# Optimization experiments

Measured on AMD Instinct MI355X. Metric: run time of the kernel, lower is better.

Reference implementation:

```python
import jax, jax.numpy as jnp
import numpy as np

# 3x3 window roll offsets, row-major as in PatchShift2D.shift_content
SHIFTS = [(1, 1), (1, 0), (1, -1), (0, 1), (0, 0), (0, -1), (-1, 1), (-1, 0), (-1, -1)]
NUM_WIN = 9


def patch_shift(x, inv):
    # x: [B, T, H, W, C]; pad C up to multiple of 9 and H,W by 1, roll each
    # of the 9 channel groups by a distinct (h, w) offset, then crop back.
    B, T, H, W, C = x.shape
    Ch = int(np.ceil(C / NUM_WIN) * NUM_WIN)
    xp = jnp.pad(x, ((0, 0), (0, 0), (1, 1), (1, 1), (0, Ch - C)))
    m = -1 if inv else 1
    parts = jnp.split(xp, NUM_WIN, axis=-1)
    shifted = [jnp.roll(p, (m * sh, m * sw), axis=(2, 3))
               for p, (sh, sw) in zip(parts, SHIFTS)]
    return jnp.concatenate(shifted, axis=-1)[:, :, 1:H + 1, 1:W + 1, :C]


def _gelu(v):
    return jax.nn.gelu(v, approximate=False)  # torch nn.GELU default (erf)


def setup_inputs() -> dict:
    key = jax.random.key(0)
    ks = jax.random.split(key, 14)
    B, T, H, W, C = 2, 8, 56, 56, 512
    HID = 1024
    s = 0.02
    return {
        "x": jax.random.normal(ks[0], (B, T, H, W, C), dtype=jnp.float32),
        "fc_w": s * jax.random.normal(ks[1], (C, HID), dtype=jnp.float32),
        "fc_b": jnp.zeros((HID,), jnp.float32),
        "fc1_w": s * jax.random.normal(ks[2], (HID, C), dtype=jnp.float32),
        "fc1_b": jnp.zeros((C,), jnp.float32),
        "fc2_w": s * jax.random.normal(ks[3], (HID, C), dtype=jnp.float32),
        "fc2_b": jnp.zeros((C,), jnp.float32),
        "rw1_w": s * jax.random.normal(ks[4], (C, C // 4), dtype=jnp.float32),
        "rw1_b": jnp.zeros((C // 4,), jnp.float32),
        "rw2_w": s * jax.random.normal(ks[5], (C // 4, 2 * C), dtype=jnp.float32),
        "rw2_b": jnp.zeros((2 * C,), jnp.float32),
        "proj_w": s * jax.random.normal(ks[6], (C, C), dtype=jnp.float32),
        "proj_b": jnp.zeros((C,), jnp.float32),
    }


def reference(x, fc_w, fc_b, fc1_w, fc1_b, fc2_w, fc2_b,
              rw1_w, rw1_b, rw2_w, rw2_b, proj_w, proj_b):
    B, T, H, W, C = x.shape
    xh = _gelu(x @ fc_w + fc_b)                                  # [B,T,H,W,HID]
    h = patch_shift(_gelu(patch_shift(xh, False) @ fc1_w + fc1_b), True)  # [B,T,H,W,C]
    w = _gelu(xh @ fc2_w + fc2_b)                                 # [B,T,H,W,C]
    a = (h + w).mean(axis=(1, 2, 3))                              # [B,C]
    a = _gelu(a @ rw1_w + rw1_b) @ rw2_w + rw2_b                  # [B,2C]
    a = jax.nn.softmax(a.reshape(B, C, 2).transpose(2, 0, 1), axis=0)  # [2,B,C]
    a = a[:, :, None, None, None, :]                              # [2,B,1,1,1,C]
    out = h * a[0] + w * a[1]
    return out @ proj_w + proj_b
```

## Files before the change

### kernel.cpp

```cpp
#include <hip/hip_runtime.h>
#include <hip/hip_bf16.h>
#include <stdint.h>


typedef __attribute__((ext_vector_type(8))) short short8;
typedef __attribute__((ext_vector_type(4))) float floatx4;
typedef unsigned int uint;
typedef unsigned short ushort;

#define NTOK   50176
#define HWIMG  3136

__device__ __align__(64) uint g_zpage[16];

__device__ __forceinline__ float gelu_exact(float v) {
    return 0.5f * v * (1.0f + erff(v * 0.70710678118654752440f));
}
__device__ __forceinline__ float gelu_fast(float v) {
    float u = v * (0.7978845608f + 0.0356774081f * v * v);
    return v * __builtin_amdgcn_rcpf(1.0f + __expf(-2.0f * u));
}

__device__ __forceinline__ int shift_h(int g) { return 1 - g / 3; }
__device__ __forceinline__ int shift_w(int g) { return 1 - g % 3; }

typedef const __attribute__((address_space(1))) uint* gas_ptr;
typedef __attribute__((address_space(3))) uint* las_ptr;

__device__ __forceinline__ void async_copy16(const void* g, void* l) {
    gas_ptr gp = (gas_ptr)(uintptr_t)g;
    las_ptr lp = (las_ptr)(uint32_t)(uintptr_t)l;
    __builtin_amdgcn_global_load_lds(gp, lp, 16, 0, 0);
}

template <int EPI, bool SHIFTA>
__global__ __launch_bounds__(256) void gemm_bt(
    const __hip_bfloat16* __restrict__ A,
    const __hip_bfloat16* __restrict__ Bt,
    const float* __restrict__ bias,
    void* __restrict__ Cout,
    float* __restrict__ ssum, int N, int K)
{
    __shared__ __align__(16) __hip_bfloat16 As[2 * 128 * 32];
    __shared__ __align__(16) __hip_bfloat16 Bs[2 * 128 * 32];

    const int t    = threadIdx.x;
    const int lane = t & 63;
    const int wave = t >> 6;
    const int wm   = wave >> 1;
    const int wn   = wave & 1;

    const int nbn  = gridDim.x;
    const int flat = blockIdx.y * nbn + blockIdx.x;
    const int xcd  = flat & 7;
    const int j    = flat >> 3;
    const int jd   = j / nbn;
    const int bm   = xcd * 49 + jd;
    const int bn   = j - jd * nbn;

    const int ar0 = bm * 128 + (t >> 2);
    const int ar1 = ar0 + 64;
    const int ac  = (t & 3) * 8;

    const __hip_bfloat16* ga0 = A  + (size_t)ar0 * K + ac;
    const __hip_bfloat16* ga1 = ga0 + (size_t)64 * K;
    const __hip_bfloat16* gb0 = Bt + (size_t)(bn * 128 + (t >> 2)) * K + ac;
    const __hip_bfloat16* gb1 = gb0 + (size_t)64 * K;

    floatx4 acc[4][4] = {};

    const int kq = (lane >> 4) * 8;
    const int ml = lane & 15;

    if constexpr (!SHIFTA) {
        auto stage = [&](int buf) {
            __hip_bfloat16* lA = &As[buf * 4096 + t * 8];
            __hip_bfloat16* lB = &Bs[buf * 4096 + t * 8];
            async_copy16(ga0, lA);
            async_copy16(ga1, lA + 2048);
            async_copy16(gb0, lB);
            async_copy16(gb1, lB + 2048);
            ga0 += 32; ga1 += 32; gb0 += 32; gb1 += 32;
        };

        const int nt = K >> 5;
        stage(0);
        for (int tt = 0; tt < nt; ++tt) {
            const int cur = tt & 1;
            if (tt + 1 < nt) {
                stage(cur ^ 1);
                asm volatile("s_waitcnt vmcnt(4)" ::: "memory");
            } else {
                asm volatile("s_waitcnt vmcnt(0)" ::: "memory");
            }
            __builtin_amdgcn_s_barrier();
            asm volatile("" ::: "memory");

            const int ab = cur * 4096;
            short8 af[4], bf[4];
#pragma unroll
            for (int i = 0; i < 4; i++) {
                af[i] = *(const short8*)&As[ab + (wm * 64 + i * 16 + ml) * 32 + kq];
                bf[i] = *(const short8*)&Bs[ab + (wn * 64 + i * 16 + ml) * 32 + kq];
            }
#pragma unroll
            for (int mi = 0; mi < 4; mi++)
#pragma unroll
                for (int ni = 0; ni < 4; ni++)
                    acc[mi][ni] = __builtin_amdgcn_mfma_f32_16x16x32_bf16(
                        af[mi], bf[ni], acc[mi][ni], 0, 0, 0);

            asm volatile("" ::: "memory");
            __builtin_amdgcn_s_barrier();
        }
    } else {
        const int rem0 = ar0 % HWIMG, rem1 = ar1 % HWIMG;
        const int oh0 = rem0 / 56, ow0 = rem0 - oh0 * 56;
        const int oh1 = rem1 / 56, ow1 = rem1 - oh1 * 56;
        const __hip_bfloat16* zsrc = (const __hip_bfloat16*)g_zpage;

        auto stageS = [&](int buf, int tx, bool& strad,
                          uint4& lo0, uint4& hi0, uint4& lo1, uint4& hi1) {
            const int c0 = tx * 32 + ac;
            const int gl = c0 / 114;
            const int gh = (c0 + 7) / 114;
            const int shl = shift_h(gl), swl = shift_w(gl);
            const int offl = shl * 56 + swl;
            const bool v0 = ((unsigned)(oh0 - shl) < 56u) && ((unsigned)(ow0 - swl) < 56u);
            const bool v1 = ((unsigned)(oh1 - shl) < 56u) && ((unsigned)(ow1 - swl) < 56u);
            strad = (gl != gh);
            const __hip_bfloat16* p0 = zsrc;
            const __hip_bfloat16* p1 = zsrc;
            if (!strad) {
                if (v0) p0 = A + (size_t)(ar0 - offl) * K + c0;
                if (v1) p1 = A + (size_t)(ar1 - offl) * K + c0;
            } else {
                const int shh = shift_h(gh), swh = shift_w(gh);
                const int offh = shh * 56 + swh;
                const bool w0 = ((unsigned)(oh0 - shh) < 56u) && ((unsigned)(ow0 - swh) < 56u);
                const bool w1 = ((unsigned)(oh1 - shh) < 56u) && ((unsigned)(ow1 - swh) < 56u);
                lo0 = *(const uint4*)(A + (size_t)(ar0 - (v0 ? offl : 0)) * K + c0);
                hi0 = *(const uint4*)(A + (size_t)(ar0 - (w0 ? offh : 0)) * K + c0);
                lo1 = *(const uint4*)(A + (size_t)(ar1 - (v1 ? offl : 0)) * K + c0);
                hi1 = *(const uint4*)(A + (size_t)(ar1 - (w1 ? offh : 0)) * K + c0);
            }
            async_copy16(p0, &As[buf * 4096 + t * 8]);
            async_copy16(p1, &As[buf * 4096 + t * 8 + 2048]);
            async_copy16(gb0, &Bs[buf * 4096 + t * 8]);
            async_copy16(gb1, &Bs[buf * 4096 + t * 8 + 2048]);
            gb0 += 32; gb1 += 32;
        };

        auto mergeS = [&](int buf, int tx,
                          const uint4& lo0, const uint4& hi0,
                          const uint4& lo1, const uint4& hi1) {
            const int c0 = tx * 32 + ac;
            const int gl = c0 / 114;
            const int gh = (c0 + 7) / 114;
            if (gl == gh) return;
            const int shl = shift_h(gl), swl = shift_w(gl);
            const int shh = shift_h(gh), swh = shift_w(gh);
            const bool v0 = ((unsigned)(oh0 - shl) < 56u) && ((unsigned)(ow0 - swl) < 56u);
            const bool v1 = ((unsigned)(oh1 - shl) < 56u) && ((unsigned)(ow1 - swl) < 56u);
            const bool w0 = ((unsigned)(oh0 - shh) < 56u) && ((unsigned)(ow0 - swh) < 56u);
            const bool w1 = ((unsigned)(oh1 - shh) < 56u) && ((unsigned)(ow1 - swh) < 56u);
            const int thr = (gl + 1) * 114 - c0;
            const uint ml0 = v0 ? ~0u : 0u, mh0 = w0 ? ~0u : 0u;
            const uint ml1 = v1 ? ~0u : 0u, mh1 = w1 ? ~0u : 0u;
            auto mw = [&](uint lo, uint hi, uint mlo, uint mhi, int jb) -> uint {
                const uint l = lo & mlo, h = hi & mhi;
                const uint e0 = (jb < thr)     ? (l & 0xffffu)      : (h & 0xffffu);
                const uint e1 = (jb + 1 < thr) ? (l & 0xffff0000u)  : (h & 0xffff0000u);
                return e0 | e1;
            };
            uint4 m0, m1;
            m0.x = mw(lo0.x, hi0.x, ml0, mh0, 0);
            m0.y = mw(lo0.y, hi0.y, ml0, mh0, 2);
            m0.z = mw(lo0.z, hi0.z, ml0, mh0, 4);
            m0.w = mw(lo0.w, hi0.w, ml0, mh0, 6);
            m1.x = mw(lo1.x, hi1.x, ml1, mh1, 0);
            m1.y = mw(lo1.y, hi1.y, ml1, mh1, 2);
            m1.z = mw(lo1.z, hi1.z, ml1, mh1, 4);
            m1.w = mw(lo1.w, hi1.w, ml1, mh1, 6);
            *(uint4*)&As[buf * 4096 + t * 8]        = m0;
            *(uint4*)&As[buf * 4096 + t * 8 + 2048] = m1;
        };

        const int nt = K >> 5;
        uint4 plo0, phi0, plo1, phi1;
        bool strad0;
        stageS(0, 0, strad0, plo0, phi0, plo1, phi1);

        for (int tt = 0; tt < nt; ++tt) {
            const int cur = tt & 1;
            uint4 nlo0, nhi0, nlo1, nhi1;
            bool nstrad = false;
            if (tt + 1 < nt) {
                stageS(cur ^ 1, tt + 1, nstrad, nlo0, nhi0, nlo1, nhi1);
                asm volatile("s_waitcnt vmcnt(4)" ::: "memory");
            } else {
                asm volatile("s_waitcnt vmcnt(0)" ::: "memory");
            }
            mergeS(cur, tt, plo0, phi0, plo1, phi1);
            asm volatile("s_waitcnt lgkmcnt(0)" ::: "memory");
            __builtin_amdgcn_s_barrier();
            asm volatile("" ::: "memory");

            const int ab = cur * 4096;
            short8 af[4], bf[4];
#pragma unroll
            for (int i = 0; i < 4; i++) {
                af[i] = *(const short8*)&As[ab + (wm * 64 + i * 16 + ml) * 32 + kq];
                bf[i] = *(const short8*)&Bs[ab + (wn * 64 + i * 16 + ml) * 32 + kq];
            }
#pragma unroll
            for (int mi = 0; mi < 4; mi++)
#pragma unroll
                for (int ni = 0; ni < 4; ni++)
                    acc[mi][ni] = __builtin_amdgcn_mfma_f32_16x16x32_bf16(
                        af[mi], bf[ni], acc[mi][ni], 0, 0, 0);

            asm volatile("" ::: "memory");
            __builtin_amdgcn_s_barrier();
            if (nstrad) { plo0 = nlo0; phi0 = nhi0; plo1 = nlo1; phi1 = nhi1; }
        }
    }

    const int rq = (lane >> 4) * 4;

    int cols[4], gsh[4], gsw[4];
    float bv[4];
    float sum[4] = {0.f, 0.f, 0.f, 0.f};
#pragma unroll
    for (int ni = 0; ni < 4; ni++) {
        const int col = bn * 128 + wn * 64 + ni * 16 + ml;
        cols[ni] = col;
        bv[ni] = bias[col];
        if (EPI == 2) { const int g = col / 57; gsh[ni] = shift_h(g); gsw[ni] = shift_w(g); }
    }

#pragma unroll
    for (int mi = 0; mi < 4; mi++) {
        const int row0 = bm * 128 + wm * 64 + mi * 16 + rq;
        int phr[4], pwr[4];
        if (EPI == 2) {
            const int bt_ = row0 / HWIMG;
            const int rem = row0 - bt_ * HWIMG;
            const int ph0 = rem / 56;
            const int pw0 = rem - ph0 * 56;
#pragma unroll
            for (int r = 0; r < 4; r++) {
                int pw = pw0 + r, ph = ph0;
                if (pw >= 56) { pw -= 56; ph += 1; }
                if (ph >= 56) { ph = 0; }
                phr[r] = ph; pwr[r] = pw;
            }
        }
#pragma unroll
        for (int ni = 0; ni < 4; ni++) {
            const int col = cols[ni];
#pragma unroll
            for (int r = 0; r < 4; r++) {
                const int tok = row0 + r;
                float v = acc[mi][ni][r] + bv[ni];
                if (EPI != 0) v = gelu_fast(v);
                if (EPI == 0) {
                    ((float*)Cout)[(size_t)tok * N + col] = v;
                } else if (EPI == 1) {
                    ((__hip_bfloat16*)Cout)[(size_t)tok * N + col] = __float2bfloat16(v);
                } else if (EPI == 2) {
                    const int th = phr[r] - gsh[ni], tw = pwr[r] - gsw[ni];
                    if ((unsigned)th < 56u && (unsigned)tw < 56u) {
                        ((__hip_bfloat16*)Cout)[(size_t)(tok - gsh[ni] * 56 - gsw[ni]) * N + col]
                            = __float2bfloat16(v);
                        sum[ni] += v;
                    }
                } else {
                    ((__hip_bfloat16*)Cout)[(size_t)tok * N + col] = __float2bfloat16(v);
                    sum[ni] += v;
                }
            }
        }
    }

    if (EPI == 2 || EPI == 3) {
        const int b = (bm >= 196) ? 1 : 0;
#pragma unroll
        for (int ni = 0; ni < 4; ni++) {
            float s = sum[ni];
            s += __shfl_xor(s, 16, 64);
            s += __shfl_xor(s, 32, 64);
            if (lane < 16) atomicAdd(&ssum[b * 512 + cols[ni]], s);
        }
    }
}

template <int C, int GS, int SGN>
__global__ __launch_bounds__(256) void zero_holes(__hip_bfloat16* __restrict__ buf)
{
    const int i = blockIdx.x * 256 + threadIdx.x;
    const int c = i % C;
    const int p = i / C;
    const int bt = p / 220, fp = p % 220;
    int oh, ow;
    if (fp < 56)       { oh = 0;        ow = fp; }
    else if (fp < 112) { oh = 55;       ow = fp - 56; }
    else if (fp < 166) { oh = fp - 111; ow = 0; }
    else               { oh = fp - 165; ow = 55; }
    const int g = c / GS;
    const int ih = oh - SGN * shift_h(g);
    const int iw = ow - SGN * shift_w(g);
    if ((unsigned)ih >= 56u || (unsigned)iw >= 56u)
        buf[((size_t)(bt * HWIMG + oh * 56 + ow)) * C + c] = __float2bfloat16(0.0f);
}

__global__ __launch_bounds__(256) void cvt_x(const float4* __restrict__ x,
                                             __hip_bfloat16* __restrict__ xb)
{
    int i = blockIdx.x * 256 + threadIdx.x;
    float4 v = x[i];
    __hip_bfloat16 b0 = __float2bfloat16(v.x);
    __hip_bfloat16 b1 = __float2bfloat16(v.y);
    __hip_bfloat16 b2 = __float2bfloat16(v.z);
    __hip_bfloat16 b3 = __float2bfloat16(v.w);
    uint2 o;
    o.x = (uint)*(ushort*)&b0 | ((uint)*(ushort*)&b1 << 16);
    o.y = (uint)*(ushort*)&b2 | ((uint)*(ushort*)&b3 << 16);
    *(uint2*)&xb[(size_t)i * 4] = o;
}

__global__ __launch_bounds__(256) void prep_w(
    const float* __restrict__ fcw,  const float* __restrict__ fc1w,
    const float* __restrict__ fc2w, const float* __restrict__ projw,
    __hip_bfloat16* __restrict__ fcwT, __hip_bfloat16* __restrict__ fc1T,
    __hip_bfloat16* __restrict__ fc2T, __hip_bfloat16* __restrict__ projT)
{
    int i = blockIdx.x * 256 + threadIdx.x;
    if (i < 524288) {
        int n = i >> 9, k = i & 511;
        fcwT[i] = __float2bfloat16(fcw[k * 1024 + n]);
    } else if (i < 1048576) {
        int j = i - 524288;
        int n = j >> 10, k = j & 1023;
        fc1T[j] = __float2bfloat16(fc1w[k * 512 + n]);
    } else if (i < 1572864) {
        int j = i - 1048576;
        int n = j >> 10, k = j & 1023;
        fc2T[j] = __float2bfloat16(fc2w[k * 512 + n]);
    } else if (i < 1835008) {
        int j = i - 1572864;
        int n = j >> 9, k = j & 511;
        projT[j] = __float2bfloat16(projw[k * 512 + n]);
    }
}

__global__ __launch_bounds__(256) void tiny_mlp(
    const float* __restrict__ s0, const float* __restrict__ s1,
    const float* __restrict__ rw1_w, const float* __restrict__ rw1_b,
    const float* __restrict__ rw2_w, const float* __restrict__ rw2_b,
    float* __restrict__ a0, float* __restrict__ a1)
{
    __shared__ float mean[1024];
    __shared__ float z[256];
    __shared__ float av[2048];
    const int t = threadIdx.x;
    for (int i = t; i < 1024; i += 256)
        mean[i] = (s0[i] + s1[i]) * (1.0f / 25088.0f);
    __syncthreads();
    {
        const int b = t >> 7, j = t & 127;
        float acc = rw1_b[j];
        for (int cc = 0; cc < 512; cc++)
            acc += mean[b * 512 + cc] * rw1_w[cc * 128 + j];
        z[t] = gelu_exact(acc);
    }
    __syncthreads();
    for (int i = t; i < 2048; i += 256) {
        const int b = i >> 10, o = i & 1023;
        float acc = rw2_b[o];
        for (int j = 0; j < 128; j++)
            acc += z[b * 128 + j] * rw2_w[j * 1024 + o];
        av[i] = acc;
    }
    __syncthreads();
    for (int i = t; i < 1024; i += 256) {
        const int b = i >> 9, cc = i & 511;
        const float x0 = av[b * 1024 + 2 * cc];
        const float x1 = av[b * 1024 + 2 * cc + 1];
        const float m = fmaxf(x0, x1);
        const float e0 = expf(x0 - m), e1 = expf(x1 - m);
        const float inv = 1.0f / (e0 + e1);
        a0[i] = e0 * inv;
        a1[i] = e1 * inv;
    }
}

__device__ __forceinline__ float bf_lo(uint u) { return __uint_as_float(u << 16); }
__device__ __forceinline__ float bf_hi(uint u) { return __uint_as_float(u & 0xffff0000u); }
__device__ __forceinline__ uint pack_bf2(float lo, float hi) {
    __hip_bfloat16 a = __float2bfloat16(lo), b = __float2bfloat16(hi);
    return (uint)*(ushort*)&a | ((uint)*(ushort*)&b << 16);
}

__global__ __launch_bounds__(256) void combine(
    const uint4* __restrict__ hs4, const uint4* __restrict__ w4,
    const float* __restrict__ a0, const float* __restrict__ a1,
    uint4* __restrict__ hw4)
{
    const int i = blockIdx.x * 256 + threadIdx.x;
    const int ck = i & 63;
    const int tok = i >> 6;
    const int b = (tok >= 25088) ? 1 : 0;
    const float4* A0 = (const float4*)&a0[b * 512 + ck * 8];
    const float4* A1 = (const float4*)&a1[b * 512 + ck * 8];
    const float4 s0l = A0[0], s0h = A0[1];
    const float4 s1l = A1[0], s1h = A1[1];
    const uint4 h = hs4[i], w = w4[i];
    uint4 o;
    o.x = pack_bf2(bf_lo(h.x) * s0l.x + bf_lo(w.x) * s1l.x,
                   bf_hi(h.x) * s0l.y + bf_hi(w.x) * s1l.y);
    o.y = pack_bf2(bf_lo(h.y) * s0l.z + bf_lo(w.y) * s1l.z,
                   bf_hi(h.y) * s0l.w + bf_hi(w.y) * s1l.w);
    o.z = pack_bf2(bf_lo(h.z) * s0h.x + bf_lo(w.z) * s1h.x,
                   bf_hi(h.z) * s0h.y + bf_hi(w.z) * s1h.y);
    o.w = pack_bf2(bf_lo(h.w) * s0h.z + bf_lo(w.w) * s1h.z,
                   bf_hi(h.w) * s0h.w + bf_hi(w.w) * s1h.w);
    hw4[i] = o;
}

extern "C" void kernel_launch(void* const* d_in, const int* in_sizes, int n_in,
                              void* d_out, int out_size, void* d_ws, size_t ws_size,
                              hipStream_t stream)
{
    const float* x      = (const float*)d_in[0];
    const float* fc_w   = (const float*)d_in[1];
    const float* fc_b   = (const float*)d_in[2];
    const float* fc1_w  = (const float*)d_in[3];
    const float* fc1_b  = (const float*)d_in[4];
    const float* fc2_w  = (const float*)d_in[5];
    const float* fc2_b  = (const float*)d_in[6];
    const float* rw1_w  = (const float*)d_in[7];
    const float* rw1_b  = (const float*)d_in[8];
    const float* rw2_w  = (const float*)d_in[9];
    const float* rw2_b  = (const float*)d_in[10];
    const float* proj_w = (const float*)d_in[11];
    const float* proj_b = (const float*)d_in[12];

    uint8_t* ws = (uint8_t*)d_ws;
    __hip_bfloat16* xh  = (__hip_bfloat16*)(ws);
    __hip_bfloat16* xb  = (__hip_bfloat16*)(ws + 102760448);
    uint8_t* wt         = ws + 102760448 + 51380224;
    __hip_bfloat16* fcwT  = (__hip_bfloat16*)(wt);
    __hip_bfloat16* fc1T  = fcwT + 524288;
    __hip_bfloat16* fc2T  = fc1T + 524288;
    __hip_bfloat16* projT = fc2T + 524288;
    float* s0 = (float*)(wt + 3670016);
    float* s1 = s0 + 1024;
    float* a0 = s1 + 1024;
    float* a1 = a0 + 1024;

    __hip_bfloat16* wbuf = (__hip_bfloat16*)d_out;
    __hip_bfloat16* hs   = xb;
    __hip_bfloat16* hw   = xh;

    hipMemsetAsync(s0, 0, 8192, stream);

    cvt_x<<<25088, 256, 0, stream>>>((const float4*)x, xb);
    prep_w<<<7168, 256, 0, stream>>>(fc_w, fc1_w, fc2_w, proj_w, fcwT, fc1T, fc2T, projT);

    gemm_bt<1, false><<<dim3(8, 392), 256, 0, stream>>>(
        xb, fcwT, fc_b, xh, nullptr, 1024, 512);
    zero_holes<512, 57, -1><<<7040, 256, 0, stream>>>(hs);
    gemm_bt<2, true><<<dim3(4, 392), 256, 0, stream>>>(
        xh, fc1T, fc1_b, hs, s0, 512, 1024);
    gemm_bt<3, false><<<dim3(4, 392), 256, 0, stream>>>(
        xh, fc2T, fc2_b, wbuf, s1, 512, 1024);
    tiny_mlp<<<1, 256, 0, stream>>>(s0, s1, rw1_w, rw1_b, rw2_w, rw2_b, a0, a1);
    combine<<<12544, 256, 0, stream>>>((const uint4*)hs, (const uint4*)wbuf, a0, a1, (uint4*)hw);
    gemm_bt<0, false><<<dim3(4, 392), 256, 0, stream>>>(
        hw, projT, proj_b, d_out, nullptr, 512, 512);
}
```

Before: 566.2 us.

## Deepen GEMM LDS pipeline from double to triple buffering

Grows the shared-memory A/B tiles from two stages to three and prefetches two k-tiles ahead in both the plain and the shifted-A GEMM paths. Wait counts and the rotation of register-held straddle data are changed to match. The aim is to hide global-load latency behind more MFMA work. In exchange, LDS use and register pressure rise, which may reduce occupancy. The merge guard now depends on the straddle flag, so correctness relies on mergeS being a no-op when that flag is false.

```diff
diff --git a/kernel.cpp b/kernel.cpp
--- a/kernel.cpp
+++ b/kernel.cpp
@@ -41,8 +41,8 @@
     void* __restrict__ Cout,
     float* __restrict__ ssum, int N, int K)
 {
-    __shared__ __align__(16) __hip_bfloat16 As[2 * 128 * 32];
-    __shared__ __align__(16) __hip_bfloat16 Bs[2 * 128 * 32];
+    __shared__ __align__(16) __hip_bfloat16 As[3 * 128 * 32];
+    __shared__ __align__(16) __hip_bfloat16 Bs[3 * 128 * 32];
 
     const int t    = threadIdx.x;
     const int lane = t & 63;
@@ -85,10 +85,15 @@
 
         const int nt = K >> 5;
         stage(0);
+        stage(1);
+        int nb = 2;
         for (int tt = 0; tt < nt; ++tt) {
-            const int cur = tt & 1;
-            if (tt + 1 < nt) {
-                stage(cur ^ 1);
+            const int cur = tt - (tt / 3) * 3;
+            if (tt + 2 < nt) {
+                stage(nb);
+                nb = (nb == 2) ? 0 : nb + 1;
+                asm volatile("s_waitcnt vmcnt(8)" ::: "memory");
+            } else if (tt + 1 < nt) {
                 asm volatile("s_waitcnt vmcnt(4)" ::: "memory");
             } else {
                 asm volatile("s_waitcnt vmcnt(0)" ::: "memory");
@@ -187,21 +192,27 @@
         };
 
         const int nt = K >> 5;
-        uint4 plo0, phi0, plo1, phi1;
-        bool strad0;
-        stageS(0, 0, strad0, plo0, phi0, plo1, phi1);
-
+        uint4 al0, ah0, al1, ah1;
+        uint4 bl0, bh0, bl1, bh1;
+        uint4 cl0, ch0, cl1, ch1;
+        bool sa, sb, sc;
+        stageS(0, 0, sa, al0, ah0, al1, ah1);
+        stageS(1, 1, sb, bl0, bh0, bl1, bh1);
+        int nb = 2;
         for (int tt = 0; tt < nt; ++tt) {
-            const int cur = tt & 1;
-            uint4 nlo0, nhi0, nlo1, nhi1;
-            bool nstrad = false;
-            if (tt + 1 < nt) {
-                stageS(cur ^ 1, tt + 1, nstrad, nlo0, nhi0, nlo1, nhi1);
+            const int cur = tt - (tt / 3) * 3;
+            bool staged = false;
+            if (tt + 2 < nt) {
+                stageS(nb, tt + 2, sc, cl0, ch0, cl1, ch1);
+                nb = (nb == 2) ? 0 : nb + 1;
+                staged = true;
+                asm volatile("s_waitcnt vmcnt(8)" ::: "memory");
+            } else if (tt + 1 < nt) {
                 asm volatile("s_waitcnt vmcnt(4)" ::: "memory");
             } else {
                 asm volatile("s_waitcnt vmcnt(0)" ::: "memory");
             }
-            mergeS(cur, tt, plo0, phi0, plo1, phi1);
+            if (sa) mergeS(cur, tt, al0, ah0, al1, ah1);
             asm volatile("s_waitcnt lgkmcnt(0)" ::: "memory");
             __builtin_amdgcn_s_barrier();
             asm volatile("" ::: "memory");
@@ -222,7 +233,8 @@
 
             asm volatile("" ::: "memory");
             __builtin_amdgcn_s_barrier();
-            if (nstrad) { plo0 = nlo0; phi0 = nhi0; plo1 = nlo1; phi1 = nhi1; }
+            al0 = bl0; ah0 = bh0; al1 = bl1; ah1 = bh1; sa = sb;
+            if (staged) { bl0 = cl0; bh0 = ch0; bl1 = cl1; bh1 = ch1; sb = sc; }
         }
     }
 
```

New measurement: 582.7 us. 1.03x slower.
